# Kernel optimization log

Hardware: AMD Instinct MI355X
Metric: run time of the kernel (lower is better)

Reference implementation:

```python
import jax, jax.numpy as jnp
import numpy as np

NEG_INF = -1e10
EPSILON = 1e-10
BLOCK = 32  # KV block size from init (block_size=32)


def setup_inputs() -> dict:
    key = jax.random.key(0)
    k1, k2, k3 = jax.random.split(key, 3)
    B, L, H, D = 4, 2048, 16, 64
    return {
        "queries": jax.random.normal(k1, (B, L, H, D), dtype=jnp.float32),
        "keys": jax.random.normal(k2, (B, L, H, D), dtype=jnp.float32),
        "values": jax.random.normal(k3, (B, L, H, D), dtype=jnp.float32),
    }


def _flash_attn(queries, keys, values):
    # [B, L, H, D] -> [B, H, L, D]
    Q = jnp.transpose(queries, (0, 2, 1, 3))
    K = jnp.transpose(keys, (0, 2, 1, 3))
    V = jnp.transpose(values, (0, 2, 1, 3))
    B, H, L, D = Q.shape
    scale = 1.0 / np.sqrt(D).astype(np.float32)
    Tc = L // BLOCK
    # Stack KV blocks along a leading scan axis: [Tc, B, H, BLOCK, D]
    Kb = jnp.moveaxis(K.reshape(B, H, Tc, BLOCK, D), 2, 0)
    Vb = jnp.moveaxis(V.reshape(B, H, Tc, BLOCK, D), 2, 0)
    Qs = Q * scale

    O0 = jnp.zeros_like(Q)
    l0 = jnp.zeros((B, H, L, 1), dtype=Q.dtype)
    m0 = jnp.full((B, H, L, 1), NEG_INF, dtype=Q.dtype)

    def step(carry, kv):
        O, l, m = carry
        Kj, Vj = kv
        # S: [B, H, L, BLOCK]
        S = jnp.einsum("bhid,bhjd->bhij", Qs, Kj)
        m_blk = jnp.max(S, axis=-1, keepdims=True)
        P = jnp.exp(S - m_blk)
        l_blk = jnp.sum(P, axis=-1, keepdims=True) + EPSILON  # per-block epsilon, as in source
        PV = jnp.einsum("bhij,bhjd->bhid", P, Vj)
        m_new = jnp.maximum(m_blk, m)
        l_new = jnp.exp(m - m_new) * l + jnp.exp(m_blk - m_new) * l_blk
        O_new = l / l_new * jnp.exp(m - m_new) * O + jnp.exp(m_blk - m_new) / l_new * PV
        return (O_new, l_new, m_new), None

    (O, _, _), _ = jax.lax.scan(step, (O0, l0, m0), (Kb, Vb))
    # back to [B, L, H, D]
    return jnp.transpose(O, (0, 2, 1, 3))


def reference(queries, keys, values):
    return _flash_attn(queries, keys, values)
```

## Files before the change

kernel.cpp:

```cpp
#include <hip/hip_runtime.h>
#include <hip/hip_bf16.h>

typedef float f32x4 __attribute__((ext_vector_type(4)));
typedef float f32x16 __attribute__((ext_vector_type(16)));
typedef short s16x8 __attribute__((ext_vector_type(8)));
typedef unsigned u32x2 __attribute__((ext_vector_type(2)));

#define L_C 2048
#define H_C 16
#define D_C 64
#define SL  1024
#define KVBLK 64
#define NT (L_C / KVBLK)
#define TILE_B 8192

__device__ __forceinline__ unsigned f2bf_u(float f) {
  union { float f; unsigned u; } v; v.f = f;
  return (v.u + 0x7fffu + ((v.u >> 16) & 1u)) >> 16;
}
__device__ __forceinline__ uint2 pack4(float a, float b, float c, float d) {
  uint2 u;
  u.x = f2bf_u(a) | (f2bf_u(b) << 16);
  u.y = f2bf_u(c) | (f2bf_u(d) << 16);
  return u;
}

__device__ __forceinline__ unsigned cvtpk(float lo, float hi) {
  unsigned r;
  asm("v_cvt_pk_bf16_f32 %0, %1, %2" : "=v"(r) : "v"(lo), "v"(hi));
  return r;
}
__device__ __forceinline__ void p32swap(unsigned &a, unsigned &b) {
  u32x2 r = __builtin_amdgcn_permlane32_swap(a, b, false, false);
  a = r[0]; b = r[1];
}
__device__ __forceinline__ float xhi_max(float x) {
  unsigned a = __float_as_uint(x), b = a;
  u32x2 r = __builtin_amdgcn_permlane32_swap(a, b, false, false);
  return fmaxf(__uint_as_float(r[0]), __uint_as_float(r[1]));
}
__device__ __forceinline__ float xhi_add(float x) {
  unsigned a = __float_as_uint(x), b = a;
  u32x2 r = __builtin_amdgcn_permlane32_swap(a, b, false, false);
  return __uint_as_float(r[0]) + __uint_as_float(r[1]);
}

__device__ __forceinline__ void packPB(const f32x16 &S, s16x8 &fa, s16x8 &fb) {
  unsigned W0 = cvtpk(S[0], S[1]),  W1 = cvtpk(S[2], S[3]);
  unsigned W2 = cvtpk(S[4], S[5]),  W3 = cvtpk(S[6], S[7]);
  unsigned W4 = cvtpk(S[8], S[9]),  W5 = cvtpk(S[10], S[11]);
  unsigned W6 = cvtpk(S[12], S[13]), W7 = cvtpk(S[14], S[15]);
  p32swap(W0, W2); p32swap(W1, W3); p32swap(W4, W6); p32swap(W5, W7);
  union { unsigned u[4]; s16x8 s; } A, B;
  A.u[0] = W0; A.u[1] = W1; A.u[2] = W2; A.u[3] = W3;
  B.u[0] = W4; B.u[1] = W5; B.u[2] = W6; B.u[3] = W7;
  fa = A.s; fb = B.s;
}

#define GLDS16(g, l) __builtin_amdgcn_global_load_lds(                          \
    (const __attribute__((address_space(1))) unsigned int*)(g),                 \
    (__attribute__((address_space(3))) unsigned int*)(l), 16, 0, 0)

__global__ __launch_bounds__(256) void convKV(const float* __restrict__ K,
                                              const float* __restrict__ V,
                                              unsigned short* __restrict__ Kw,
                                              unsigned short* __restrict__ Vw) {
  const int bid = blockIdx.x;
  const int bh = bid >> 5, t = bid & 31;
  const int b = bh >> 4, h = bh & 15;
  const int tid = threadIdx.x;

  {
    const float* src = K + ((size_t)b * L_C * SL) + h * D_C;
    char* dst = (char*)Kw + (size_t)bid * TILE_B;
#pragma unroll
    for (int j = 0; j < 2; ++j) {
      const int u = tid + j * 256;
      const int fi = u >> 6, l = u & 63;
      const int cb = fi >> 2, kc = fi & 3;
      const float* p = src + (size_t)(t * 64 + cb * 32 + (l & 31)) * SL +
                       kc * 16 + (l >> 5) * 8;
      float4 x = *(const float4*)p;
      float4 y = *(const float4*)(p + 4);
      union { unsigned u[4]; s16x8 s; } cv;
      cv.u[0] = cvtpk(x.x, x.y); cv.u[1] = cvtpk(x.z, x.w);
      cv.u[2] = cvtpk(y.x, y.y); cv.u[3] = cvtpk(y.z, y.w);
      *(s16x8*)(dst + u * 16) = cv.s;
    }
  }
  {
    const float* src = V + ((size_t)b * L_C * SL) + h * D_C;
    char* dst = (char*)Vw + (size_t)bid * TILE_B;
    const int d = (tid >> 3) * 2;
    const int c8 = tid & 7;
    const int kc = c8 >> 1, hi = c8 & 1;
    const float* p = src + (size_t)(t * 64 + c8 * 8) * SL + d;
    float2 v[8];
#pragma unroll
    for (int k = 0; k < 8; ++k) v[k] = *(const float2*)(p + (size_t)k * SL);
    union { unsigned u[4]; s16x8 s; } c0, c1;
    c0.u[0] = cvtpk(v[0].x, v[1].x); c0.u[1] = cvtpk(v[2].x, v[3].x);
    c0.u[2] = cvtpk(v[4].x, v[5].x); c0.u[3] = cvtpk(v[6].x, v[7].x);
    c1.u[0] = cvtpk(v[0].y, v[1].y); c1.u[1] = cvtpk(v[2].y, v[3].y);
    c1.u[2] = cvtpk(v[4].y, v[5].y); c1.u[3] = cvtpk(v[6].y, v[7].y);
    const int db = d >> 5;
    const int l0 = hi * 32 + (d & 31);
    *(s16x8*)(dst + (size_t)((db * 4 + kc) * 64 + l0) * 16) = c0.s;
    *(s16x8*)(dst + (size_t)((db * 4 + kc) * 64 + l0 + 1) * 16) = c1.s;
  }
}

__global__ __launch_bounds__(256) void fattn3(
    const float* __restrict__ Qg, const unsigned short* __restrict__ Kw,
    const unsigned short* __restrict__ Vw, float* __restrict__ Og) {
  __shared__ __align__(16) unsigned short Klds[2][4096];
  __shared__ __align__(16) unsigned short Vlds[2][4096];

  const int gid = blockIdx.x;
  const int swz = (gid & 7) * 128 + (gid >> 3);
  const int bh = swz >> 4, qt = swz & 15;
  const int b = bh >> 4, h = bh & 15;

  const int tid = threadIdx.x;
  const int w = tid >> 6;
  const int lane = tid & 63;
  const int hi = lane >> 5;
  const int lq = lane & 31;

  const float* Qb = Qg + ((size_t)b * L_C * SL) + h * D_C;
  float*       Ob = Og + ((size_t)b * L_C * SL) + h * D_C;
  const char* Ktile = (const char*)(Kw + (size_t)bh * 32 * 4096);
  const char* Vtile = (const char*)(Vw + (size_t)bh * 32 * 4096);

  const int q0 = qt * 128 + w * 32;
  const int soff = w * 2048;
  const int slane = soff + lane * 16;

  GLDS16(Ktile + slane, (char*)Klds[0] + soff);
  GLDS16(Ktile + slane + 1024, (char*)Klds[0] + soff + 1024);
  GLDS16(Vtile + slane, (char*)Vlds[0] + soff);
  GLDS16(Vtile + slane + 1024, (char*)Vlds[0] + soff + 1024);

  const float QS = 0.125f * 1.44269504088896340736f;
  s16x8 qf[4];
  {
    const float* qrow = Qb + (size_t)(q0 + lq) * SL + hi * 8;
#pragma unroll
    for (int kc = 0; kc < 4; ++kc) {
      float4 x = *(const float4*)(qrow + kc * 16);
      float4 y = *(const float4*)(qrow + kc * 16 + 4);
      union { unsigned u[4]; s16x8 s; } cv;
      cv.u[0] = cvtpk(x.x * QS, x.y * QS); cv.u[1] = cvtpk(x.z * QS, x.w * QS);
      cv.u[2] = cvtpk(y.x * QS, y.y * QS); cv.u[3] = cvtpk(y.z * QS, y.w * QS);
      qf[kc] = cv.s;
    }
  }

  f32x16 Ot0, Ot1;
#pragma unroll
  for (int i = 0; i < 16; ++i) { Ot0[i] = 0.f; Ot1[i] = 0.f; }
  float mS = -1e30f, lS = 0.f;

  __syncthreads();
  int cur = 0;

  for (int t = 0; t < NT; ++t) {
    if (t + 1 < NT) {
      const char* kt = Ktile + (size_t)(t + 1) * TILE_B;
      const char* vt = Vtile + (size_t)(t + 1) * TILE_B;
      char* kd = (char*)Klds[cur ^ 1] + soff;
      char* vd = (char*)Vlds[cur ^ 1] + soff;
      GLDS16(kt + slane, kd);
      GLDS16(kt + slane + 1024, kd + 1024);
      GLDS16(vt + slane, vd);
      GLDS16(vt + slane + 1024, vd + 1024);
    }
    const char* Kc = (const char*)Klds[cur];
    const char* Vc = (const char*)Vlds[cur];
    const int lo16 = lane * 16;

    f32x16 S0, S1;
#pragma unroll
    for (int i = 0; i < 16; ++i) { S0[i] = 0.f; S1[i] = 0.f; }
#pragma unroll
    for (int kc = 0; kc < 4; ++kc) {
      s16x8 kf = *(const s16x8*)(Kc + kc * 1024 + lo16);
      S0 = __builtin_amdgcn_mfma_f32_32x32x16_bf16(kf, qf[kc], S0, 0, 0, 0);
    }
#pragma unroll
    for (int kc = 0; kc < 4; ++kc) {
      s16x8 kf = *(const s16x8*)(Kc + (4 + kc) * 1024 + lo16);
      S1 = __builtin_amdgcn_mfma_f32_32x32x16_bf16(kf, qf[kc], S1, 0, 0, 0);
    }

    float mb = fmaxf(S0[0], S0[1]);
#pragma unroll
    for (int r = 2; r < 16; ++r) mb = fmaxf(mb, S0[r]);
#pragma unroll
    for (int r = 0; r < 16; ++r) mb = fmaxf(mb, S1[r]);
    mb = xhi_max(mb);

    if (!__all(mb <= mS + 8.0f)) {
      const float mnew = fmaxf(mS, mb);
      const float al = __builtin_amdgcn_exp2f(mS - mnew);
      lS *= al;
#pragma unroll
      for (int r = 0; r < 16; ++r) { Ot0[r] *= al; Ot1[r] *= al; }
      mS = mnew;
    }
    float ps = 0.f;
#pragma unroll
    for (int r = 0; r < 16; ++r) {
      S0[r] = __builtin_amdgcn_exp2f(S0[r] - mS); ps += S0[r];
    }
#pragma unroll
    for (int r = 0; r < 16; ++r) {
      S1[r] = __builtin_amdgcn_exp2f(S1[r] - mS); ps += S1[r];
    }
    lS += xhi_add(ps);

    s16x8 pf0, pf1, pf2, pf3;
    packPB(S0, pf0, pf1);
    packPB(S1, pf2, pf3);

#pragma unroll
    for (int kc = 0; kc < 4; ++kc) {
      s16x8 vf = *(const s16x8*)(Vc + kc * 1024 + lo16);
      s16x8 pf = (kc == 0) ? pf0 : (kc == 1) ? pf1 : (kc == 2) ? pf2 : pf3;
      Ot0 = __builtin_amdgcn_mfma_f32_32x32x16_bf16(vf, pf, Ot0, 0, 0, 0);
    }
#pragma unroll
    for (int kc = 0; kc < 4; ++kc) {
      s16x8 vf = *(const s16x8*)(Vc + (4 + kc) * 1024 + lo16);
      s16x8 pf = (kc == 0) ? pf0 : (kc == 1) ? pf1 : (kc == 2) ? pf2 : pf3;
      Ot1 = __builtin_amdgcn_mfma_f32_32x32x16_bf16(vf, pf, Ot1, 0, 0, 0);
    }

    __syncthreads();
    cur ^= 1;
  }

  const float inv = 1.0f / lS;
  float* orow = Ob + (size_t)(q0 + lq) * SL;
#pragma unroll
  for (int r = 0; r < 16; ++r) {
    const int d = (r & 3) + 8 * (r >> 2) + 4 * hi;
    orow[d] = Ot0[r] * inv;
    orow[32 + d] = Ot1[r] * inv;
  }
}

__global__ __launch_bounds__(256) void fattn_fb(
    const float* __restrict__ Qg, const float* __restrict__ Kg,
    const float* __restrict__ Vg, float* __restrict__ Og) {
  __shared__ unsigned short Klds[64 * 64];
  __shared__ unsigned short Vlds[64 * 64];
  __shared__ unsigned short Plds[4 * 16 * 64];

  const int gid = blockIdx.x;
  const int swz = (gid & 7) * 128 + (gid >> 3);
  const int bh = swz >> 4, qt = swz & 15;
  const int b = bh >> 4, h = bh & 15;

  const int tid = threadIdx.x;
  const int w = tid >> 6;
  const int lane = tid & 63;
  const int lg = lane >> 4;
  const int lr = lane & 15;

  const float* Qb = Qg + ((size_t)b * L_C * SL) + h * D_C;
  const float* Kb = Kg + ((size_t)b * L_C * SL) + h * D_C;
  const float* Vb = Vg + ((size_t)b * L_C * SL) + h * D_C;
  float*       Ob = Og + ((size_t)b * L_C * SL) + h * D_C;

  const int q0 = qt * 128 + w * 32;
  const float QS = 0.125f * 1.44269504088896340736f;
  s16x8 qf[2][2];
#pragma unroll
  for (int s = 0; s < 2; ++s) {
    const float* qp = Qb + (size_t)(q0 + s * 16 + lr) * SL + lg * 8;
#pragma unroll
    for (int kc = 0; kc < 2; ++kc) {
      float4 x = *(const float4*)(qp + kc * 32);
      float4 y = *(const float4*)(qp + kc * 32 + 4);
      s16x8 tq;
      tq[0] = (short)f2bf_u(x.x * QS); tq[1] = (short)f2bf_u(x.y * QS);
      tq[2] = (short)f2bf_u(x.z * QS); tq[3] = (short)f2bf_u(x.w * QS);
      tq[4] = (short)f2bf_u(y.x * QS); tq[5] = (short)f2bf_u(y.y * QS);
      tq[6] = (short)f2bf_u(y.z * QS); tq[7] = (short)f2bf_u(y.w * QS);
      qf[s][kc] = tq;
    }
  }

  f32x4 Oa[2][4];
#pragma unroll
  for (int s = 0; s < 2; ++s)
#pragma unroll
    for (int df = 0; df < 4; ++df) Oa[s][df] = f32x4{0.f, 0.f, 0.f, 0.f};
  float m_s[2] = {-1e30f, -1e30f};
  float l_s[2] = {0.f, 0.f};

  char* pb = (char*)Plds + w * 2048 + lr * 128;
  const int psw = (lr & 7) << 4;

  for (int t = 0; t < NT; ++t) {
    const int kv0 = t * KVBLK;
    __syncthreads();
    {
      const int r = tid >> 2, c = tid & 3;
      const float* kp = Kb + (size_t)(kv0 + r) * SL;
      char* krow = (char*)Klds + r * 128;
      const int sw = (r & 7) << 4;
#pragma unroll
      for (int i = 0; i < 4; ++i) {
        const int f4 = c + 4 * i;
        float4 x = *(const float4*)(kp + f4 * 4);
        *(uint2*)(krow + ((f4 * 8) ^ sw)) = pack4(x.x, x.y, x.z, x.w);
      }
    }
    {
      const int rq = tid >> 4, dq = tid & 15;
      const float* vp = Vb + (size_t)(kv0 + rq * 4) * SL + dq * 4;
      float4 v0 = *(const float4*)(vp);
      float4 v1 = *(const float4*)(vp + SL);
      float4 v2 = *(const float4*)(vp + 2 * SL);
      float4 v3 = *(const float4*)(vp + 3 * SL);
      const float* p0 = (const float*)&v0; const float* p1 = (const float*)&v1;
      const float* p2 = (const float*)&v2; const float* p3 = (const float*)&v3;
#pragma unroll
      for (int dd = 0; dd < 4; ++dd) {
        const int row = dq * 4 + dd;
        *(uint2*)((char*)Vlds + row * 128 + ((rq * 8) ^ ((row & 7) << 4))) =
            pack4(p0[dd], p1[dd], p2[dd], p3[dd]);
      }
    }
    __syncthreads();

    s16x8 kf[4][2];
#pragma unroll
    for (int f = 0; f < 4; ++f) {
      const int row = f * 16 + lr;
      char* kr = (char*)Klds + row * 128;
      const int sw = (row & 7) << 4;
      kf[f][0] = *(const s16x8*)(kr + ((lg * 16) ^ sw));
      kf[f][1] = *(const s16x8*)(kr + ((lg * 16 + 64) ^ sw));
    }

#pragma unroll
    for (int s = 0; s < 2; ++s) {
      f32x4 Sf[4];
#pragma unroll
      for (int f = 0; f < 4; ++f) Sf[f] = f32x4{0.f, 0.f, 0.f, 0.f};
#pragma unroll
      for (int f = 0; f < 4; ++f)
#pragma unroll
        for (int kc = 0; kc < 2; ++kc)
          Sf[f] = __builtin_amdgcn_mfma_f32_16x16x32_bf16(kf[f][kc], qf[s][kc],
                                                          Sf[f], 0, 0, 0);
      float mb = Sf[0][0];
#pragma unroll
      for (int f = 0; f < 4; ++f)
#pragma unroll
        for (int r = 0; r < 4; ++r) mb = fmaxf(mb, Sf[f][r]);
      mb = fmaxf(mb, __shfl_xor(mb, 16, 64));
      mb = fmaxf(mb, __shfl_xor(mb, 32, 64));
      const float mnew = fmaxf(m_s[s], mb);
      const float al = __builtin_amdgcn_exp2f(m_s[s] - mnew);
      float ps = 0.f;
#pragma unroll
      for (int f = 0; f < 4; ++f)
#pragma unroll
        for (int r = 0; r < 4; ++r) {
          float p = __builtin_amdgcn_exp2f(Sf[f][r] - mnew);
          Sf[f][r] = p;
          ps += p;
        }
      ps += __shfl_xor(ps, 16, 64);
      ps += __shfl_xor(ps, 32, 64);
      l_s[s] = l_s[s] * al + ps;
      m_s[s] = mnew;

      float alr[4];
#pragma unroll
      for (int r = 0; r < 4; ++r) alr[r] = __shfl(al, lg * 4 + r, 64);
#pragma unroll
      for (int df = 0; df < 4; ++df)
#pragma unroll
        for (int r = 0; r < 4; ++r) Oa[s][df][r] *= alr[r];

#pragma unroll
      for (int f = 0; f < 4; ++f)
        *(uint2*)(pb + ((f * 32 + lg * 8) ^ psw)) =
            pack4(Sf[f][0], Sf[f][1], Sf[f][2], Sf[f][3]);
      asm volatile("s_waitcnt lgkmcnt(0)" ::: "memory");
      s16x8 pa0 = *(const s16x8*)(pb + ((lg * 16) ^ psw));
      s16x8 pa1 = *(const s16x8*)(pb + ((lg * 16 + 64) ^ psw));
#pragma unroll
      for (int df = 0; df < 4; ++df) {
        const int row = df * 16 + lr;
        char* vr = (char*)Vlds + row * 128;
        const int sw = (row & 7) << 4;
        s16x8 vf0 = *(const s16x8*)(vr + ((lg * 16) ^ sw));
        s16x8 vf1 = *(const s16x8*)(vr + ((lg * 16 + 64) ^ sw));
        Oa[s][df] = __builtin_amdgcn_mfma_f32_16x16x32_bf16(pa0, vf0, Oa[s][df], 0, 0, 0);
        Oa[s][df] = __builtin_amdgcn_mfma_f32_16x16x32_bf16(pa1, vf1, Oa[s][df], 0, 0, 0);
      }
    }
  }

#pragma unroll
  for (int s = 0; s < 2; ++s) {
    float li[4];
#pragma unroll
    for (int r = 0; r < 4; ++r) li[r] = 1.0f / __shfl(l_s[s], lg * 4 + r, 64);
#pragma unroll
    for (int r = 0; r < 4; ++r) {
      float* op = Ob + (size_t)(q0 + s * 16 + lg * 4 + r) * SL + lr;
#pragma unroll
      for (int df = 0; df < 4; ++df) op[df * 16] = Oa[s][df][r] * li[r];
    }
  }
}

extern "C" void kernel_launch(void* const* d_in, const int* in_sizes, int n_in,
                              void* d_out, int out_size, void* d_ws, size_t ws_size,
                              hipStream_t stream) {
  const float* Q = (const float*)d_in[0];
  const float* K = (const float*)d_in[1];
  const float* V = (const float*)d_in[2];
  float* O = (float*)d_out;
  const size_t elems = (size_t)64 * 32 * 4096;
  const size_t need = elems * 2 * 2;
  if (ws_size >= need) {
    unsigned short* Kw = (unsigned short*)d_ws;
    unsigned short* Vw = Kw + elems;
    convKV<<<dim3(2048), dim3(256), 0, stream>>>(K, V, Kw, Vw);
    fattn3<<<dim3(1024), dim3(256), 0, stream>>>(Q, Kw, Vw, O);
  } else {
    fattn_fb<<<dim3(1024), dim3(256), 0, stream>>>(Q, K, V, O);
  }
}
```

Before: 123.2 us.

## Double block to 512 threads, interleave MFMA chains, use tree reductions and setprio

Each workgroup now has 8 waves covering 256 query rows, so every K/V tile loaded into LDS serves twice as many queries and each thread issues a single global-to-LDS load per tile. The two independent S and O MFMA chains are interleaved and wrapped in s_setprio to raise wave priority around matrix ops. The row max uses 3-input max trees and the row sum uses a pairwise tree, both to shorten dependency chains. The larger block may reduce occupancy and lengthens barrier waits.

```diff
diff --git a/kernel.cpp b/kernel.cpp
--- a/kernel.cpp
+++ b/kernel.cpp
@@ -43,6 +43,9 @@
   unsigned a = __float_as_uint(x), b = a;
   u32x2 r = __builtin_amdgcn_permlane32_swap(a, b, false, false);
   return __uint_as_float(r[0]) + __uint_as_float(r[1]);
+}
+__device__ __forceinline__ float fmax3(float a, float b, float c) {
+  return fmaxf(fmaxf(a, b), c);
 }
 
 __device__ __forceinline__ void packPB(const f32x16 &S, s16x8 &fa, s16x8 &fb) {
@@ -110,15 +113,15 @@
   }
 }
 
-__global__ __launch_bounds__(256) void fattn3(
+__global__ __launch_bounds__(512) void fattn4(
     const float* __restrict__ Qg, const unsigned short* __restrict__ Kw,
     const unsigned short* __restrict__ Vw, float* __restrict__ Og) {
   __shared__ __align__(16) unsigned short Klds[2][4096];
   __shared__ __align__(16) unsigned short Vlds[2][4096];
 
   const int gid = blockIdx.x;
-  const int swz = (gid & 7) * 128 + (gid >> 3);
-  const int bh = swz >> 4, qt = swz & 15;
+  const int swz = (gid & 7) * 64 + (gid >> 3);
+  const int bh = swz >> 3, qt = swz & 7;
   const int b = bh >> 4, h = bh & 15;
 
   const int tid = threadIdx.x;
@@ -132,14 +135,12 @@
   const char* Ktile = (const char*)(Kw + (size_t)bh * 32 * 4096);
   const char* Vtile = (const char*)(Vw + (size_t)bh * 32 * 4096);
 
-  const int q0 = qt * 128 + w * 32;
-  const int soff = w * 2048;
+  const int q0 = qt * 256 + w * 32;
+  const int soff = w * 1024;
   const int slane = soff + lane * 16;
 
   GLDS16(Ktile + slane, (char*)Klds[0] + soff);
-  GLDS16(Ktile + slane + 1024, (char*)Klds[0] + soff + 1024);
   GLDS16(Vtile + slane, (char*)Vlds[0] + soff);
-  GLDS16(Vtile + slane + 1024, (char*)Vlds[0] + soff + 1024);
 
   const float QS = 0.125f * 1.44269504088896340736f;
   s16x8 qf[4];
@@ -156,49 +157,65 @@
     }
   }
 
-  f32x16 Ot0, Ot1;
-#pragma unroll
-  for (int i = 0; i < 16; ++i) { Ot0[i] = 0.f; Ot1[i] = 0.f; }
+  f32x16 Zv;
+#pragma unroll
+  for (int i = 0; i < 16; ++i) Zv[i] = 0.f;
+  f32x16 Ot0 = Zv, Ot1 = Zv;
   float mS = -1e30f, lS = 0.f;
+
+  const char* kt = Ktile + TILE_B + slane;
+  const char* vt = Vtile + TILE_B + slane;
 
   __syncthreads();
   int cur = 0;
 
   for (int t = 0; t < NT; ++t) {
     if (t + 1 < NT) {
-      const char* kt = Ktile + (size_t)(t + 1) * TILE_B;
-      const char* vt = Vtile + (size_t)(t + 1) * TILE_B;
       char* kd = (char*)Klds[cur ^ 1] + soff;
       char* vd = (char*)Vlds[cur ^ 1] + soff;
-      GLDS16(kt + slane, kd);
-      GLDS16(kt + slane + 1024, kd + 1024);
-      GLDS16(vt + slane, vd);
-      GLDS16(vt + slane + 1024, vd + 1024);
+      GLDS16(kt, kd);
+      GLDS16(vt, vd);
+      kt += TILE_B; vt += TILE_B;
     }
     const char* Kc = (const char*)Klds[cur];
     const char* Vc = (const char*)Vlds[cur];
     const int lo16 = lane * 16;
 
     f32x16 S0, S1;
-#pragma unroll
-    for (int i = 0; i < 16; ++i) { S0[i] = 0.f; S1[i] = 0.f; }
-#pragma unroll
-    for (int kc = 0; kc < 4; ++kc) {
-      s16x8 kf = *(const s16x8*)(Kc + kc * 1024 + lo16);
-      S0 = __builtin_amdgcn_mfma_f32_32x32x16_bf16(kf, qf[kc], S0, 0, 0, 0);
-    }
-#pragma unroll
-    for (int kc = 0; kc < 4; ++kc) {
-      s16x8 kf = *(const s16x8*)(Kc + (4 + kc) * 1024 + lo16);
-      S1 = __builtin_amdgcn_mfma_f32_32x32x16_bf16(kf, qf[kc], S1, 0, 0, 0);
-    }
-
-    float mb = fmaxf(S0[0], S0[1]);
-#pragma unroll
-    for (int r = 2; r < 16; ++r) mb = fmaxf(mb, S0[r]);
-#pragma unroll
-    for (int r = 0; r < 16; ++r) mb = fmaxf(mb, S1[r]);
-    mb = xhi_max(mb);
+    {
+      s16x8 kf0 = *(const s16x8*)(Kc + 0 * 1024 + lo16);
+      s16x8 kf4 = *(const s16x8*)(Kc + 4 * 1024 + lo16);
+      __builtin_amdgcn_s_setprio(1);
+      S0 = __builtin_amdgcn_mfma_f32_32x32x16_bf16(kf0, qf[0], Zv, 0, 0, 0);
+      S1 = __builtin_amdgcn_mfma_f32_32x32x16_bf16(kf4, qf[0], Zv, 0, 0, 0);
+      __builtin_amdgcn_s_setprio(0);
+    }
+#pragma unroll
+    for (int kc = 1; kc < 4; ++kc) {
+      s16x8 kfa = *(const s16x8*)(Kc + kc * 1024 + lo16);
+      s16x8 kfb = *(const s16x8*)(Kc + (4 + kc) * 1024 + lo16);
+      __builtin_amdgcn_s_setprio(1);
+      S0 = __builtin_amdgcn_mfma_f32_32x32x16_bf16(kfa, qf[kc], S0, 0, 0, 0);
+      S1 = __builtin_amdgcn_mfma_f32_32x32x16_bf16(kfb, qf[kc], S1, 0, 0, 0);
+      __builtin_amdgcn_s_setprio(0);
+    }
+
+    float a0 = fmax3(S0[0],  S0[1],  S0[2]);
+    float a1 = fmax3(S0[3],  S0[4],  S0[5]);
+    float a2 = fmax3(S0[6],  S0[7],  S0[8]);
+    float a3 = fmax3(S0[9],  S0[10], S0[11]);
+    float a4 = fmax3(S0[12], S0[13], S0[14]);
+    float a5 = fmax3(S0[15], S1[0],  S1[1]);
+    float a6 = fmax3(S1[2],  S1[3],  S1[4]);
+    float a7 = fmax3(S1[5],  S1[6],  S1[7]);
+    float a8 = fmax3(S1[8],  S1[9],  S1[10]);
+    float a9 = fmax3(S1[11], S1[12], S1[13]);
+    float aA = fmaxf(S1[14], S1[15]);
+    float b0 = fmax3(a0, a1, a2);
+    float b1 = fmax3(a3, a4, a5);
+    float b2 = fmax3(a6, a7, a8);
+    float b3 = fmax3(a9, aA, b0);
+    float mb = xhi_max(fmax3(b1, b2, b3));
 
     if (!__all(mb <= mS + 8.0f)) {
       const float mnew = fmaxf(mS, mb);
@@ -208,15 +225,23 @@
       for (int r = 0; r < 16; ++r) { Ot0[r] *= al; Ot1[r] *= al; }
       mS = mnew;
     }
-    float ps = 0.f;
-#pragma unroll
-    for (int r = 0; r < 16; ++r) {
-      S0[r] = __builtin_amdgcn_exp2f(S0[r] - mS); ps += S0[r];
-    }
-#pragma unroll
-    for (int r = 0; r < 16; ++r) {
-      S1[r] = __builtin_amdgcn_exp2f(S1[r] - mS); ps += S1[r];
-    }
+#pragma unroll
+    for (int r = 0; r < 16; ++r) S0[r] = __builtin_amdgcn_exp2f(S0[r] - mS);
+#pragma unroll
+    for (int r = 0; r < 16; ++r) S1[r] = __builtin_amdgcn_exp2f(S1[r] - mS);
+
+    float u[16];
+#pragma unroll
+    for (int i = 0; i < 8; ++i) u[i] = S0[2 * i] + S0[2 * i + 1];
+#pragma unroll
+    for (int i = 0; i < 8; ++i) u[8 + i] = S1[2 * i] + S1[2 * i + 1];
+    float v8[8];
+#pragma unroll
+    for (int i = 0; i < 8; ++i) v8[i] = u[2 * i] + u[2 * i + 1];
+    float w4[4];
+#pragma unroll
+    for (int i = 0; i < 4; ++i) w4[i] = v8[2 * i] + v8[2 * i + 1];
+    float ps = (w4[0] + w4[1]) + (w4[2] + w4[3]);
     lS += xhi_add(ps);
 
     s16x8 pf0, pf1, pf2, pf3;
@@ -225,15 +250,13 @@
 
 #pragma unroll
     for (int kc = 0; kc < 4; ++kc) {
-      s16x8 vf = *(const s16x8*)(Vc + kc * 1024 + lo16);
+      s16x8 vfa = *(const s16x8*)(Vc + kc * 1024 + lo16);
+      s16x8 vfb = *(const s16x8*)(Vc + (4 + kc) * 1024 + lo16);
       s16x8 pf = (kc == 0) ? pf0 : (kc == 1) ? pf1 : (kc == 2) ? pf2 : pf3;
-      Ot0 = __builtin_amdgcn_mfma_f32_32x32x16_bf16(vf, pf, Ot0, 0, 0, 0);
-    }
-#pragma unroll
-    for (int kc = 0; kc < 4; ++kc) {
-      s16x8 vf = *(const s16x8*)(Vc + (4 + kc) * 1024 + lo16);
-      s16x8 pf = (kc == 0) ? pf0 : (kc == 1) ? pf1 : (kc == 2) ? pf2 : pf3;
-      Ot1 = __builtin_amdgcn_mfma_f32_32x32x16_bf16(vf, pf, Ot1, 0, 0, 0);
+      __builtin_amdgcn_s_setprio(1);
+      Ot0 = __builtin_amdgcn_mfma_f32_32x32x16_bf16(vfa, pf, Ot0, 0, 0, 0);
+      Ot1 = __builtin_amdgcn_mfma_f32_32x32x16_bf16(vfb, pf, Ot1, 0, 0, 0);
+      __builtin_amdgcn_s_setprio(0);
     }
 
     __syncthreads();
@@ -435,7 +458,7 @@
     unsigned short* Kw = (unsigned short*)d_ws;
     unsigned short* Vw = Kw + elems;
     convKV<<<dim3(2048), dim3(256), 0, stream>>>(K, V, Kw, Vw);
-    fattn3<<<dim3(1024), dim3(256), 0, stream>>>(Q, Kw, Vw, O);
+    fattn4<<<dim3(512), dim3(512), 0, stream>>>(Q, Kw, Vw, O);
   } else {
     fattn_fb<<<dim3(1024), dim3(256), 0, stream>>>(Q, K, V, O);
   }
```

Measured after the change: 113.3 us. 8.1% less time.
